# Optimization experiments

Measured on AMD Instinct MI355X. Metric: run time of the kernel, lower is better.

The kernel has to match this reference:

```python
import jax, jax.numpy as jnp
import numpy as np

FEAT = 256
HID = FEAT // 2
N_KEYS = 2          # output_keys = ["energy_0", "energy_1"]
N_MOLS = 2000
ATOMS_PER_MOL = 100
N_ATOMS = N_MOLS * ATOMS_PER_MOL
LOG2 = 0.6931471805599453


def shifted_softplus(x):
    # NFF's shifted softplus: softplus(x) - log(2)
    return jax.nn.softplus(x) - LOG2


def setup_inputs() -> dict:
    key = jax.random.key(0)
    ks = jax.random.split(key, 6)
    s_i = jax.random.normal(ks[0], (N_ATOMS, FEAT), dtype=jnp.float32)
    xyz = jax.random.normal(ks[1], (N_ATOMS, 3), dtype=jnp.float32)
    num_atoms = jnp.full((N_MOLS,), ATOMS_PER_MOL, dtype=jnp.int64)
    # Per-key MLP params stacked over keys: Linear(F->H), act, Linear(H->1)
    W1 = jax.random.normal(ks[2], (N_KEYS, FEAT, HID), dtype=jnp.float32) / np.sqrt(FEAT)
    b1 = jnp.zeros((N_KEYS, HID), dtype=jnp.float32)
    W2 = jax.random.normal(ks[3], (N_KEYS, HID), dtype=jnp.float32) / np.sqrt(HID)
    b2 = jnp.zeros((N_KEYS,), dtype=jnp.float32)
    return {"s_i": s_i, "xyz": xyz, "num_atoms": num_atoms,
            "W1": W1, "b1": b1, "W2": W2, "b2": b2}


def reference(s_i, xyz, num_atoms, W1, b1, W2, b2):
    n_mols = num_atoms.shape[0]
    # segment id per atom, replacing the torch.split(...)+per-chunk sum loop
    seg = jnp.repeat(jnp.arange(n_mols), num_atoms,
                     total_repeat_length=s_i.shape[0])        # [N]
    # per-key MLP: [K,N,H] hidden, [K,N] scalar output per atom
    h = shifted_softplus(jnp.einsum('nf,kfh->knh', s_i, W1) + b1[:, None, :])
    val = jnp.einsum('knh,kh->kn', h, W2) + b2[:, None]       # [K, N]
    # fused segment-sum pooling -> per-molecule scalars
    pooled = jax.ops.segment_sum(val.T, seg, num_segments=n_mols)  # [M, K]
    return pooled.T                                            # [K, M]
```

## Files before the change

### kernel.cpp

```cpp
#include <hip/hip_runtime.h>

#define FEAT 256
#define HID 128
#define NKEYS 2

typedef __bf16 bf16x8 __attribute__((ext_vector_type(8)));
typedef float f32x16 __attribute__((ext_vector_type(16)));

union Frag {
    bf16x8 v;
    unsigned u[4];
    uint4 q;
};

__device__ __forceinline__ unsigned pack_bf16_2(float f0, float f1) {
    unsigned u0 = __float_as_uint(f0) + 0x8000u;
    unsigned u1 = __float_as_uint(f1) + 0x8000u;
    return __builtin_amdgcn_perm(u1, u0, 0x07060302u);
}

__device__ __forceinline__ float ssp(float x) {
    float sp = __logf(1.0f + __expf(x));
    sp = (x > 15.0f) ? x : sp;
    return sp - 0.69314718056f;
}

__device__ __forceinline__ int find_mol(const int* __restrict__ off, int n_mols, int g) {
    int lo = 0, hi = n_mols;
    while (hi - lo > 1) {
        int mid = (lo + hi) >> 1;
        if (off[mid] <= g) lo = mid; else hi = mid;
    }
    return lo;
}

__global__ void prep_kernel(const void* __restrict__ num_atoms_raw,
                            const float* __restrict__ W1,
                            int n_mols, int n_atoms,
                            int* __restrict__ off,
                            unsigned short* __restrict__ Bp,
                            float* __restrict__ out, int out_n) {
    if (blockIdx.x > 0) {
        int idx = (blockIdx.x - 1) * 256 + threadIdx.x;
        int c = idx >> 8;
        int k = idx & 255;
        int key = c >> 7, j = c & 127;
        float f = W1[(size_t)key * FEAT * HID + (size_t)k * HID + j];
        unsigned u = __float_as_uint(f);
        unsigned r = (u + 0x7FFFu + ((u >> 16) & 1u)) >> 16;
        Bp[(size_t)c * FEAT + k] = (unsigned short)r;
        return;
    }
    for (int i = threadIdx.x; i < out_n; i += 256) out[i] = 0.0f;

    __shared__ long long tsum[256];
    __shared__ int csum[257];
    __shared__ int mode_sh;
    int tid = threadIdx.x;
    const int* a32 = (const int*)num_atoms_raw;
    const long long* a64 = (const long long*)num_atoms_raw;
    int chunk = (n_mols + 255) >> 8;
    int lo = tid * chunk;
    if (lo > n_mols) lo = n_mols;
    int hi = lo + chunk;
    if (hi > n_mols) hi = n_mols;
    long long s = 0;
    for (int i = lo; i < hi; ++i) s += (long long)a32[i];
    tsum[tid] = s;
    __syncthreads();
    if (tid == 0) {
        long long t = 0;
        for (int i = 0; i < 256; ++i) t += tsum[i];
        mode_sh = (t == (long long)n_atoms) ? 0 : 1;
    }
    __syncthreads();
    int mode = mode_sh;
    if (mode) {
        s = 0;
        for (int i = lo; i < hi; ++i) s += a64[i];
        tsum[tid] = s;
    }
    csum[tid] = (int)tsum[tid];
    __syncthreads();
    if (tid == 0) {
        int run = 0;
        for (int i = 0; i < 256; ++i) { int v = csum[i]; csum[i] = run; run += v; }
    }
    __syncthreads();
    int run = csum[tid];
    for (int i = lo; i < hi; ++i) {
        off[i] = run;
        run += mode ? (int)a64[i] : a32[i];
    }
    if (hi >= n_mols) off[n_mols] = run;
}

__global__ __launch_bounds__(256, 2)
void gemm_fused(const float* __restrict__ A,
                const unsigned short* __restrict__ Bp,
                const float* __restrict__ b1,
                const float* __restrict__ W2,
                const float* __restrict__ b2,
                const int* __restrict__ off,
                float* __restrict__ out,
                int n_atoms, int n_mols) {
    __shared__ uint4 ldsA[64 * 8];
    __shared__ float part[4][64];
    __shared__ float molacc[NKEYS][4];

    const int tid  = threadIdx.x;
    const int lane = tid & 63;
    const int wn   = tid >> 6;
    const int l31  = lane & 31;
    const int half = lane >> 5;
    const int m0   = blockIdx.x * 64;

    const int srow = tid >> 2;
    const int sseg = tid & 3;
    int grow = m0 + srow;
    if (grow > n_atoms - 1) grow = n_atoms - 1;
    const float4* gsrc = (const float4*)(A + (size_t)grow * FEAT + sseg * 16);
    const int wu0 = srow * 8 + (((sseg * 2)    ) ^ (srow & 7));
    const int wu1 = srow * 8 + (((sseg * 2) + 1) ^ (srow & 7));

    const int c0 = wn * 64 + l31;
    const unsigned short* bb0 = Bp + (size_t)c0 * FEAT + half * 8;
    const unsigned short* bb1 = Bp + (size_t)(c0 + 32) * FEAT + half * 8;
    const int rbase0 = l31 * 8;
    const int rbase1 = (l31 + 32) * 8;
    const int rxor = l31 & 7;

    f32x16 acc00 = 0.0f, acc01 = 0.0f, acc10 = 0.0f, acc11 = 0.0f;

    #pragma unroll
    for (int c = 0; c < FEAT / 64; ++c) {
        const int kb = c * 64;
        Frag bf0[4], bf1[4];
        #pragma unroll
        for (int j = 0; j < 4; ++j) {
            bf0[j].q = *(const uint4*)(bb0 + kb + j * 16);
            bf1[j].q = *(const uint4*)(bb1 + kb + j * 16);
        }
        float4 f0 = gsrc[c * 16 + 0];
        float4 f1 = gsrc[c * 16 + 1];
        float4 f2 = gsrc[c * 16 + 2];
        float4 f3 = gsrc[c * 16 + 3];
        if (c > 0) __syncthreads();
        uint4 p0, p1;
        p0.x = pack_bf16_2(f0.x, f0.y);
        p0.y = pack_bf16_2(f0.z, f0.w);
        p0.z = pack_bf16_2(f1.x, f1.y);
        p0.w = pack_bf16_2(f1.z, f1.w);
        p1.x = pack_bf16_2(f2.x, f2.y);
        p1.y = pack_bf16_2(f2.z, f2.w);
        p1.z = pack_bf16_2(f3.x, f3.y);
        p1.w = pack_bf16_2(f3.z, f3.w);
        ldsA[wu0] = p0;
        ldsA[wu1] = p1;
        __syncthreads();

        #pragma unroll
        for (int j = 0; j < 4; ++j) {
            const int u = j * 2 + half;
            const int sw = u ^ rxor;
            Frag a0, a1;
            a0.q = ldsA[rbase0 + sw];
            a1.q = ldsA[rbase1 + sw];
            acc00 = __builtin_amdgcn_mfma_f32_32x32x16_bf16(a0.v, bf0[j].v, acc00, 0, 0, 0);
            acc01 = __builtin_amdgcn_mfma_f32_32x32x16_bf16(a0.v, bf1[j].v, acc01, 0, 0, 0);
            acc10 = __builtin_amdgcn_mfma_f32_32x32x16_bf16(a1.v, bf0[j].v, acc10, 0, 0, 0);
            acc11 = __builtin_amdgcn_mfma_f32_32x32x16_bf16(a1.v, bf1[j].v, acc11, 0, 0, 0);
        }
    }

    if (tid < NKEYS * 4) molacc[tid >> 2][tid & 3] = 0.0f;

    float b1c0 = b1[c0], b1c1 = b1[c0 + 32];
    float w2c0 = W2[c0], w2c1 = W2[c0 + 32];

    #pragma unroll
    for (int rt = 0; rt < 2; ++rt) {
        const f32x16& Ac0 = rt ? acc10 : acc00;
        const f32x16& Ac1 = rt ? acc11 : acc01;
        #pragma unroll
        for (int r = 0; r < 16; ++r) {
            float t = ssp(Ac0[r] + b1c0) * w2c0 + ssp(Ac1[r] + b1c1) * w2c1;
            t += __shfl_xor(t, 1);
            t += __shfl_xor(t, 2);
            t += __shfl_xor(t, 4);
            t += __shfl_xor(t, 8);
            t += __shfl_xor(t, 16);
            if (l31 == r) {
                int row = rt * 32 + (r & 3) + 8 * (r >> 2) + 4 * half;
                part[wn][row] = t;
            }
        }
    }
    __syncthreads();

    if (tid < NKEYS * 64) {
        int key = tid >> 6, r = tid & 63;
        int gm = m0 + r;
        if (gm < n_atoms) {
            float val = part[2 * key][r] + part[2 * key + 1][r] + b2[key];
            int mol  = find_mol(off, n_mols, gm);
            int mol0 = find_mol(off, n_mols, m0);
            int ml = mol - mol0;
            if (ml < 4) atomicAdd(&molacc[key][ml], val);
            else        atomicAdd(&out[(size_t)key * n_mols + mol], val);
        }
    }
    __syncthreads();

    if (tid < NKEYS * 4) {
        int key = tid >> 2, ml = tid & 3;
        int mol0 = find_mol(off, n_mols, m0);
        int mol = mol0 + ml;
        if (mol < n_mols) {
            float v = molacc[key][ml];
            if (v != 0.0f) atomicAdd(&out[(size_t)key * n_mols + mol], v);
        }
    }
}

extern "C" void kernel_launch(void* const* d_in, const int* in_sizes, int n_in,
                              void* d_out, int out_size, void* d_ws, size_t ws_size,
                              hipStream_t stream) {
    const float* s_i      = (const float*)d_in[0];
    const void*  num_atoms = d_in[2];
    const float* W1 = (const float*)d_in[3];
    const float* b1 = (const float*)d_in[4];
    const float* W2 = (const float*)d_in[5];
    const float* b2 = (const float*)d_in[6];
    int n_atoms = in_sizes[0] / FEAT;
    int n_mols  = in_sizes[2];
    float* out = (float*)d_out;

    int* off = (int*)d_ws;
    size_t off_bytes = (((size_t)(n_mols + 1) * 4) + 255) & ~(size_t)255;
    unsigned short* Bp = (unsigned short*)((char*)d_ws + off_bytes);

    int pack_blocks = (NKEYS * HID * FEAT) / 256;
    prep_kernel<<<1 + pack_blocks, 256, 0, stream>>>(num_atoms, W1, n_mols, n_atoms,
                                                     off, Bp, out, out_size);

    int gblocks = (n_atoms + 63) / 64;
    gemm_fused<<<gblocks, 256, 0, stream>>>(s_i, Bp, b1, W2, b2, off, out, n_atoms, n_mols);
}
```

Baseline: 349.7 us.

## Preload full A tile into LDS once and double-buffer B fragments

After: 350.6 us. About the same (+0.3%).

```diff
diff --git a/kernel.cpp b/kernel.cpp
--- a/kernel.cpp
+++ b/kernel.cpp
@@ -104,7 +104,7 @@
                 const int* __restrict__ off,
                 float* __restrict__ out,
                 int n_atoms, int n_mols) {
-    __shared__ uint4 ldsA[64 * 8];
+    __shared__ uint4 ldsA[4 * 64 * 8];
     __shared__ float part[4][64];
     __shared__ float molacc[NKEYS][4];
 
@@ -120,32 +120,33 @@
     int grow = m0 + srow;
     if (grow > n_atoms - 1) grow = n_atoms - 1;
     const float4* gsrc = (const float4*)(A + (size_t)grow * FEAT + sseg * 16);
-    const int wu0 = srow * 8 + (((sseg * 2)    ) ^ (srow & 7));
-    const int wu1 = srow * 8 + (((sseg * 2) + 1) ^ (srow & 7));
+
+    float4 fb[16];
+    #pragma unroll
+    for (int i = 0; i < 16; ++i)
+        fb[i] = gsrc[(i >> 2) * 16 + (i & 3)];
 
     const int c0 = wn * 64 + l31;
     const unsigned short* bb0 = Bp + (size_t)c0 * FEAT + half * 8;
     const unsigned short* bb1 = Bp + (size_t)(c0 + 32) * FEAT + half * 8;
-    const int rbase0 = l31 * 8;
-    const int rbase1 = (l31 + 32) * 8;
-    const int rxor = l31 & 7;
-
-    f32x16 acc00 = 0.0f, acc01 = 0.0f, acc10 = 0.0f, acc11 = 0.0f;
-
-    #pragma unroll
-    for (int c = 0; c < FEAT / 64; ++c) {
-        const int kb = c * 64;
-        Frag bf0[4], bf1[4];
-        #pragma unroll
-        for (int j = 0; j < 4; ++j) {
-            bf0[j].q = *(const uint4*)(bb0 + kb + j * 16);
-            bf1[j].q = *(const uint4*)(bb1 + kb + j * 16);
-        }
-        float4 f0 = gsrc[c * 16 + 0];
-        float4 f1 = gsrc[c * 16 + 1];
-        float4 f2 = gsrc[c * 16 + 2];
-        float4 f3 = gsrc[c * 16 + 3];
-        if (c > 0) __syncthreads();
+    Frag bf0[2][4], bf1[2][4];
+    #pragma unroll
+    for (int j = 0; j < 4; ++j) {
+        bf0[0][j].q = *(const uint4*)(bb0 + j * 16);
+        bf1[0][j].q = *(const uint4*)(bb1 + j * 16);
+    }
+    #pragma unroll
+    for (int j = 0; j < 4; ++j) {
+        bf0[1][j].q = *(const uint4*)(bb0 + 64 + j * 16);
+        bf1[1][j].q = *(const uint4*)(bb1 + 64 + j * 16);
+    }
+
+    const int wb = srow * 8;
+    const int rx = srow & 7;
+    #pragma unroll
+    for (int c = 0; c < 4; ++c) {
+        float4 f0 = fb[c * 4 + 0], f1 = fb[c * 4 + 1];
+        float4 f2 = fb[c * 4 + 2], f3 = fb[c * 4 + 3];
         uint4 p0, p1;
         p0.x = pack_bf16_2(f0.x, f0.y);
         p0.y = pack_bf16_2(f0.z, f0.w);
@@ -155,21 +156,39 @@
         p1.y = pack_bf16_2(f2.z, f2.w);
         p1.z = pack_bf16_2(f3.x, f3.y);
         p1.w = pack_bf16_2(f3.z, f3.w);
-        ldsA[wu0] = p0;
-        ldsA[wu1] = p1;
-        __syncthreads();
-
+        ldsA[c * 512 + wb + ((sseg * 2)     ^ rx)] = p0;
+        ldsA[c * 512 + wb + ((sseg * 2 + 1) ^ rx)] = p1;
+    }
+    __syncthreads();
+
+    const int rb0 = l31 * 8;
+    const int rb1 = (l31 + 32) * 8;
+    const int rxor = l31 & 7;
+
+    f32x16 acc00 = 0.0f, acc01 = 0.0f, acc10 = 0.0f, acc11 = 0.0f;
+
+    #pragma unroll
+    for (int c = 0; c < 4; ++c) {
+        const int base = c * 512;
+        const int slot = c & 1;
         #pragma unroll
         for (int j = 0; j < 4; ++j) {
-            const int u = j * 2 + half;
-            const int sw = u ^ rxor;
+            const int sw = (j * 2 + half) ^ rxor;
             Frag a0, a1;
-            a0.q = ldsA[rbase0 + sw];
-            a1.q = ldsA[rbase1 + sw];
-            acc00 = __builtin_amdgcn_mfma_f32_32x32x16_bf16(a0.v, bf0[j].v, acc00, 0, 0, 0);
-            acc01 = __builtin_amdgcn_mfma_f32_32x32x16_bf16(a0.v, bf1[j].v, acc01, 0, 0, 0);
-            acc10 = __builtin_amdgcn_mfma_f32_32x32x16_bf16(a1.v, bf0[j].v, acc10, 0, 0, 0);
-            acc11 = __builtin_amdgcn_mfma_f32_32x32x16_bf16(a1.v, bf1[j].v, acc11, 0, 0, 0);
+            a0.q = ldsA[base + rb0 + sw];
+            a1.q = ldsA[base + rb1 + sw];
+            acc00 = __builtin_amdgcn_mfma_f32_32x32x16_bf16(a0.v, bf0[slot][j].v, acc00, 0, 0, 0);
+            acc01 = __builtin_amdgcn_mfma_f32_32x32x16_bf16(a0.v, bf1[slot][j].v, acc01, 0, 0, 0);
+            acc10 = __builtin_amdgcn_mfma_f32_32x32x16_bf16(a1.v, bf0[slot][j].v, acc10, 0, 0, 0);
+            acc11 = __builtin_amdgcn_mfma_f32_32x32x16_bf16(a1.v, bf1[slot][j].v, acc11, 0, 0, 0);
+        }
+        if (c + 2 < 4) {
+            const int kb = (c + 2) * 64;
+            #pragma unroll
+            for (int j = 0; j < 4; ++j) {
+                bf0[slot][j].q = *(const uint4*)(bb0 + kb + j * 16);
+                bf1[slot][j].q = *(const uint4*)(bb1 + kb + j * 16);
+            }
         }
     }
 
```
